# Performance work log

Measured on AMD Instinct MI355X. Metric: run time of the kernel, lower is better.

## Reference

```python
import jax, jax.numpy as jnp
import numpy as np

D_MODEL = 192
D_STATE = 16
D_CONV = 3
EXPAND = 2
D_INNER = EXPAND * D_MODEL
DT_RANK = (D_MODEL + 15) // 16  # ceil(d_model/16) = 12


def setup_inputs() -> dict:
    key = jax.random.key(0)
    ks = jax.random.split(key, 8)
    B, H, W = 4, 32, 32
    sc = lambda n: 1.0 / np.sqrt(n)
    x = jax.random.normal(ks[0], (B, H, W, D_MODEL), jnp.float32)
    W_in = jax.random.normal(ks[1], (D_MODEL, 2 * D_INNER), jnp.float32) * sc(D_MODEL)
    conv_w = jax.random.normal(ks[2], (D_INNER, 1, D_CONV, D_CONV), jnp.float32) * sc(D_CONV * D_CONV)
    conv_b = jnp.zeros((D_INNER,), jnp.float32)
    W_x = jax.random.normal(ks[3], (D_INNER, DT_RANK + 2 * D_STATE), jnp.float32) * sc(D_INNER)
    W_dt = jax.random.normal(ks[4], (DT_RANK, D_INNER), jnp.float32) * sc(DT_RANK)
    b_dt = jnp.zeros((D_INNER,), jnp.float32)
    A_log = jnp.log(jnp.tile(jnp.arange(1, D_STATE + 1, dtype=jnp.float32), (D_INNER, 1)))
    D_param = jnp.ones((D_INNER,), jnp.float32)
    W_out = jax.random.normal(ks[5], (D_INNER, D_MODEL), jnp.float32) * sc(D_INNER)
    gamma = jnp.ones((D_INNER,), jnp.float32)
    beta = jnp.zeros((D_INNER,), jnp.float32)
    return {"x": x, "W_in": W_in, "conv_w": conv_w, "conv_b": conv_b,
            "W_x": W_x, "W_dt": W_dt, "b_dt": b_dt, "A_log": A_log,
            "D_param": D_param, "W_out": W_out, "gamma": gamma, "beta": beta}


def _ssm_scan(u, W_x, W_dt, b_dt, A_log, D_param):
    # u: (B, L, D_inner). Log-cumsum closed-form linear SSM scan.
    x_dbl = u @ W_x                                   # (B,L,dt_rank+2N)
    dt = x_dbl[..., :DT_RANK]
    B_mat = x_dbl[..., DT_RANK:DT_RANK + D_STATE]     # (B,L,N)
    C_mat = x_dbl[..., DT_RANK + D_STATE:]            # (B,L,N)
    dt = jax.nn.softplus(dt @ W_dt + b_dt)            # (B,L,D)
    A = -jnp.exp(A_log)                               # (D,N)
    log_dA = jnp.einsum('bld,dn->bldn', dt, A)        # (B,L,D,N)
    dB_u = jnp.einsum('bld,bln->bldn', dt, B_mat) * u[..., None]
    log_decay = jnp.cumsum(log_dA, axis=1)
    decay = jnp.exp(log_decay)
    h = decay * jnp.cumsum(dB_u / (decay + 1e-12), axis=1)
    y = jnp.einsum('bldn,bln->bld', h, C_mat)
    return y + u * D_param


def reference(x, W_in, conv_w, conv_b, W_x, W_dt, b_dt, A_log, D_param, W_out, gamma, beta):
    B, H, W, C = x.shape
    xz = x @ W_in                                     # (B,H,W,2*D_inner)
    x_val, z = xz[..., :D_INNER], xz[..., D_INNER:]
    # depthwise 3x3 conv in NCHW
    xc = jnp.transpose(x_val, (0, 3, 1, 2))
    xc = jax.lax.conv_general_dilated(
        xc, conv_w, window_strides=(1, 1), padding='SAME',
        feature_group_count=D_INNER,
        dimension_numbers=('NCHW', 'OIHW', 'NCHW'))
    xc = xc + conv_b[None, :, None, None]
    xc = jax.nn.silu(xc)
    xv = jnp.transpose(xc, (0, 2, 3, 1))              # (B,H,W,D_inner)

    scan = lambda u: _ssm_scan(u, W_x, W_dt, b_dt, A_log, D_param)
    s1 = xv.reshape(B, H * W, D_INNER)                # row-major
    s2 = s1[:, ::-1]
    s3 = jnp.transpose(xv, (0, 2, 1, 3)).reshape(B, W * H, D_INNER)  # column-major
    s4 = s3[:, ::-1]
    y1 = scan(s1)
    y2 = scan(s2)[:, ::-1]
    y3 = scan(s3)
    y4 = scan(s4)[:, ::-1]
    # map column-major scans back to row-major order
    y3 = jnp.transpose(y3.reshape(B, W, H, D_INNER), (0, 2, 1, 3)).reshape(B, H * W, D_INNER)
    y4 = jnp.transpose(y4.reshape(B, W, H, D_INNER), (0, 2, 1, 3)).reshape(B, H * W, D_INNER)
    y = y1 + y2 + y3 + y4

    # LayerNorm over last dim (eps=1e-5)
    mu = jnp.mean(y, axis=-1, keepdims=True)
    var = jnp.mean(jnp.square(y - mu), axis=-1, keepdims=True)
    y = (y - mu) * jax.lax.rsqrt(var + 1e-5) * gamma + beta

    y = y.reshape(B, H, W, D_INNER) * jax.nn.silu(z)
    return y @ W_out
```

## Files before the change

kernel.cpp:

```cpp
#include <hip/hip_runtime.h>
#include <hip/hip_fp16.h>

#define DMODEL 192
#define DINNER 384
#define NPOS   4096
#define SEQL   1024
#define DSTATE 16
#define DTRANK 12

__device__ __forceinline__ float silu_f(float v) { return v * (1.f / (1.f + __expf(-v))); }

__device__ __forceinline__ int scan_pos(int dir, int l) {
    int s = (dir & 1) ? (SEQL - 1 - l) : l;
    return (dir & 2) ? (((s & 31) << 5) | (s >> 5)) : s;
}

__global__ void k1_inproj8(const float* __restrict__ x, const float* __restrict__ W_in,
                           float* __restrict__ x_val, float* __restrict__ gz) {
    __shared__ float xs[8 * DMODEL];
    const int t = threadIdx.x;
    const int pos0 = blockIdx.x << 3;
    for (int i = t; i < 8 * DMODEL; i += 384) xs[i] = x[pos0 * DMODEL + i];
    __syncthreads();

    float a0[8] = {0,0,0,0,0,0,0,0};
    float a1[8] = {0,0,0,0,0,0,0,0};
    for (int c = 0; c < DMODEL; ++c) {
        float w0 = W_in[c * 768 + t];
        float w1 = W_in[c * 768 + 384 + t];
#pragma unroll
        for (int g = 0; g < 8; ++g) {
            float xv = xs[g * DMODEL + c];
            a0[g] += w0 * xv;
            a1[g] += w1 * xv;
        }
    }
#pragma unroll
    for (int g = 0; g < 8; ++g) {
        x_val[(pos0 + g) * DINNER + t] = a0[g];
        gz[(pos0 + g) * DINNER + t]    = silu_f(a1[g]);
    }
}

__global__ void k2_conv(const float* __restrict__ x_val,
                        const float* __restrict__ conv_w, const float* __restrict__ conv_b,
                        const float* __restrict__ W_x,
                        __half* __restrict__ u_out, float* __restrict__ xd_out) {
    __shared__ float us[DINNER];
    __shared__ float part[8 * 44];
    const int t = threadIdx.x;
    const int pos = blockIdx.x;
    const int b = pos >> 10, hw = pos & 1023, h = hw >> 5, w = hw & 31;

    float acc = conv_b[t];
#pragma unroll
    for (int i = 0; i < 3; ++i) {
        int hh = h + i - 1;
        if (hh < 0 || hh > 31) continue;
#pragma unroll
        for (int j = 0; j < 3; ++j) {
            int ww = w + j - 1;
            if (ww < 0 || ww > 31) continue;
            acc += x_val[((b * 32 + hh) * 32 + ww) * DINNER + t] * conv_w[t * 9 + i * 3 + j];
        }
    }
    float uv = silu_f(acc);
    us[t] = uv;
    u_out[pos * DINNER + t] = __float2half(uv);
    __syncthreads();

    if (t < 352) {
        int o = t % 44, p = t / 44;
        float s = 0.f;
        int j0 = p * 48;
        for (int j = j0; j < j0 + 48; ++j) s += us[j] * W_x[j * 44 + o];
        part[p * 44 + o] = s;
    }
    __syncthreads();
    if (t < 44) {
        float s = 0.f;
#pragma unroll
        for (int p = 0; p < 8; ++p) s += part[p * 44 + t];
        xd_out[pos * 48 + t] = s;
    }
}

__global__ void k2c_dt_init(const float* __restrict__ xd, const float* __restrict__ W_dt,
                            const float* __restrict__ b_dt, const __half* __restrict__ u,
                            const float* __restrict__ Dp,
                            float* __restrict__ dt32, float* __restrict__ y_acc) {
    const int t = threadIdx.x;
    const int pos = blockIdx.x;
    const float* xr = xd + pos * 48;
    float raw = b_dt[t];
#pragma unroll
    for (int r = 0; r < DTRANK; ++r) raw += xr[r] * W_dt[r * DINNER + t];
    dt32[pos * DINNER + t] = fmaxf(raw, 0.f) + log1pf(__expf(-fabsf(raw)));

    y_acc[pos * DINNER + t] = 4.f * Dp[t] * __half2float(u[pos * DINNER + t]);
}

__global__ void k3_early(const __half* __restrict__ u, const float* __restrict__ xd,
                         const float* __restrict__ dt32, const float* __restrict__ A_log,
                         float* __restrict__ y_acc) {
    const int t = threadIdx.x;
    const int n = t & 15, dl = t >> 4;
    const int bi = blockIdx.x;
    const int chunk = bi % 24;
    const int b = (bi / 24) % 4;
    const int dir = bi / 96;
    const int d = chunk * 16 + dl;

    const float A = -__expf(A_log[d * DSTATE + n]);

    const __half* ub  = u    + b * SEQL * DINNER;
    const float* xb   = xd   + b * SEQL * 48;
    const float* dtb  = dt32 + b * SEQL * DINNER;
    float* yb = y_acc + b * SEQL * DINNER;

    float cum = 0.f, S = 0.f;
    for (int l0 = 0; l0 < SEQL; l0 += 8) {
        float dtv[8], Bv[8], Cv[8], uv[8];
        int   pk[8];
#pragma unroll
        for (int k = 0; k < 8; ++k) {
            int pos = scan_pos(dir, l0 + k);
            pk[k]  = pos;
            dtv[k] = dtb[pos * DINNER + d];
            Bv[k]  = xb[pos * 48 + DTRANK + n];
            Cv[k]  = xb[pos * 48 + DTRANK + DSTATE + n];
            uv[k]  = __half2float(ub[pos * DINNER + d]);
        }
#pragma unroll
        for (int k = 0; k < 8; ++k) {
            cum += dtv[k] * A;
            float decay = __expf(cum);
            S += (dtv[k] * Bv[k] * uv[k]) * __builtin_amdgcn_rcpf(decay + 1e-12f);
            float c = decay * S * Cv[k];
            c += __shfl_xor(c, 1);
            c += __shfl_xor(c, 2);
            c += __shfl_xor(c, 4);
            c += __shfl_xor(c, 8);
            if (n == 0) atomicAdd(&yb[pk[k] * DINNER + d], c);
        }
        if (__ballot(cum > -110.f) == 0ull) break;
    }
}

__global__ void k4_out4(const float* __restrict__ y_acc, const float* __restrict__ gz,
                        const float* __restrict__ gamma, const float* __restrict__ beta,
                        const float* __restrict__ W_out, float* __restrict__ out) {
    __shared__ float g_s[4 * DINNER];
    __shared__ float red[6];
    const int t = threadIdx.x;
    const int lane = t & 63, wave = t >> 6;
    const int pos0 = blockIdx.x << 2;

    const float g0c = gamma[t], g1c = gamma[t + 192];
    const float b0c = beta[t],  b1c = beta[t + 192];

    for (int p = 0; p < 4; ++p) {
        int pos = pos0 + p;
        float y0 = y_acc[pos * DINNER + t];
        float y1 = y_acc[pos * DINNER + t + 192];

        float s = y0 + y1;
#pragma unroll
        for (int off = 32; off > 0; off >>= 1) s += __shfl_xor(s, off);
        if (lane == 0) red[wave] = s;
        __syncthreads();
        float mu = (red[0] + red[1] + red[2]) * (1.f / 384.f);

        float d0 = y0 - mu, d1 = y1 - mu;
        float sq = d0 * d0 + d1 * d1;
#pragma unroll
        for (int off = 32; off > 0; off >>= 1) sq += __shfl_xor(sq, off);
        if (lane == 0) red[3 + wave] = sq;
        __syncthreads();
        float var = (red[3] + red[4] + red[5]) * (1.f / 384.f);
        float inv = rsqrtf(var + 1e-5f);

        g_s[p * DINNER + t]       = (d0 * inv * g0c + b0c) * gz[pos * DINNER + t];
        g_s[p * DINNER + t + 192] = (d1 * inv * g1c + b1c) * gz[pos * DINNER + t + 192];
        __syncthreads();
    }

    float acc[4] = {0.f, 0.f, 0.f, 0.f};
    for (int dd = 0; dd < DINNER; ++dd) {
        float w = W_out[dd * DMODEL + t];
#pragma unroll
        for (int p = 0; p < 4; ++p) acc[p] += g_s[p * DINNER + dd] * w;
    }
#pragma unroll
    for (int p = 0; p < 4; ++p) out[(pos0 + p) * DMODEL + t] = acc[p];
}

extern "C" void kernel_launch(void* const* d_in, const int* in_sizes, int n_in,
                              void* d_out, int out_size, void* d_ws, size_t ws_size,
                              hipStream_t stream) {
    (void)in_sizes; (void)n_in; (void)out_size; (void)ws_size;
    const float* x      = (const float*)d_in[0];
    const float* W_in   = (const float*)d_in[1];
    const float* conv_w = (const float*)d_in[2];
    const float* conv_b = (const float*)d_in[3];
    const float* W_x    = (const float*)d_in[4];
    const float* W_dt   = (const float*)d_in[5];
    const float* b_dt   = (const float*)d_in[6];
    const float* A_log  = (const float*)d_in[7];
    const float* Dp     = (const float*)d_in[8];
    const float* W_out  = (const float*)d_in[9];
    const float* gamma  = (const float*)d_in[10];
    const float* beta   = (const float*)d_in[11];

    char* base = (char*)d_ws;
    float*  R1   = (float*)base;
    __half* u    = (__half*)(base + 6291456);
    float*  xd   = (float*)(base + 9437184);
    float*  dt32 = (float*)(base + 10223616);
    float*  gz   = (float*)(base + 16515072);

    hipLaunchKernelGGL(k1_inproj8, dim3(NPOS / 8), dim3(384), 0, stream, x, W_in, R1, gz);
    hipLaunchKernelGGL(k2_conv, dim3(NPOS), dim3(384), 0, stream,
                       R1, conv_w, conv_b, W_x, u, xd);
    hipLaunchKernelGGL(k2c_dt_init, dim3(NPOS), dim3(384), 0, stream,
                       xd, W_dt, b_dt, u, Dp, dt32, R1);
    hipLaunchKernelGGL(k3_early, dim3(384), dim3(256), 0, stream,
                       u, xd, dt32, A_log, R1);
    hipLaunchKernelGGL(k4_out4, dim3(NPOS / 4), dim3(192), 0, stream,
                       R1, gz, gamma, beta, W_out, (float*)d_out);
}
```

Measured before the change: 233.1 us.

## Fuse dt/init into conv kernel, batch scan shuffles, widen output tiles

Merges the softplus dt projection and y_acc initialisation into the conv kernel, reusing the shared-memory xd row and the fp32 conv output instead of reloading from global memory, and moves y_acc to its own workspace buffer. This removes one launch and a global round-trip. The scan loop is split into phases so the exp/rcp and the cross-lane shuffle reductions for eight steps can interleave, and atomics are issued in a batch. The output kernel now handles 8 positions per block, reusing each W_out load across more rows at the cost of more registers and shared memory.

```diff
diff --git a/kernel.cpp b/kernel.cpp
--- a/kernel.cpp
+++ b/kernel.cpp
@@ -42,12 +42,15 @@
     }
 }
 
-__global__ void k2_conv(const float* __restrict__ x_val,
-                        const float* __restrict__ conv_w, const float* __restrict__ conv_b,
-                        const float* __restrict__ W_x,
-                        __half* __restrict__ u_out, float* __restrict__ xd_out) {
+__global__ void k2_conv_dt(const float* __restrict__ x_val,
+                           const float* __restrict__ conv_w, const float* __restrict__ conv_b,
+                           const float* __restrict__ W_x, const float* __restrict__ W_dt,
+                           const float* __restrict__ b_dt, const float* __restrict__ Dp,
+                           __half* __restrict__ u_out, float* __restrict__ xd_out,
+                           float* __restrict__ dt32, float* __restrict__ y_acc) {
     __shared__ float us[DINNER];
     __shared__ float part[8 * 44];
+    __shared__ float xdl[44];
     const int t = threadIdx.x;
     const int pos = blockIdx.x;
     const int b = pos >> 10, hw = pos & 1023, h = hw >> 5, w = hw & 31;
@@ -82,22 +85,16 @@
 #pragma unroll
         for (int p = 0; p < 8; ++p) s += part[p * 44 + t];
         xd_out[pos * 48 + t] = s;
-    }
-}
-
-__global__ void k2c_dt_init(const float* __restrict__ xd, const float* __restrict__ W_dt,
-                            const float* __restrict__ b_dt, const __half* __restrict__ u,
-                            const float* __restrict__ Dp,
-                            float* __restrict__ dt32, float* __restrict__ y_acc) {
-    const int t = threadIdx.x;
-    const int pos = blockIdx.x;
-    const float* xr = xd + pos * 48;
+        xdl[t] = s;
+    }
+    __syncthreads();
+
     float raw = b_dt[t];
 #pragma unroll
-    for (int r = 0; r < DTRANK; ++r) raw += xr[r] * W_dt[r * DINNER + t];
+    for (int r = 0; r < DTRANK; ++r) raw += xdl[r] * W_dt[r * DINNER + t];
     dt32[pos * DINNER + t] = fmaxf(raw, 0.f) + log1pf(__expf(-fabsf(raw)));
 
-    y_acc[pos * DINNER + t] = 4.f * Dp[t] * __half2float(u[pos * DINNER + t]);
+    y_acc[pos * DINNER + t] = 4.f * Dp[t] * uv;
 }
 
 __global__ void k3_early(const __half* __restrict__ u, const float* __restrict__ xd,
@@ -131,35 +128,44 @@
             Cv[k]  = xb[pos * 48 + DTRANK + DSTATE + n];
             uv[k]  = __half2float(ub[pos * DINNER + d]);
         }
+        float decay[8];
+#pragma unroll
+        for (int k = 0; k < 8; ++k) { cum += dtv[k] * A; decay[k] = __expf(cum); }
+        float rc[8];
+#pragma unroll
+        for (int k = 0; k < 8; ++k) rc[k] = __builtin_amdgcn_rcpf(decay[k] + 1e-12f);
+        float c[8];
 #pragma unroll
         for (int k = 0; k < 8; ++k) {
-            cum += dtv[k] * A;
-            float decay = __expf(cum);
-            S += (dtv[k] * Bv[k] * uv[k]) * __builtin_amdgcn_rcpf(decay + 1e-12f);
-            float c = decay * S * Cv[k];
-            c += __shfl_xor(c, 1);
-            c += __shfl_xor(c, 2);
-            c += __shfl_xor(c, 4);
-            c += __shfl_xor(c, 8);
-            if (n == 0) atomicAdd(&yb[pk[k] * DINNER + d], c);
+            S += (dtv[k] * Bv[k] * uv[k]) * rc[k];
+            c[k] = decay[k] * S * Cv[k];
+        }
+#pragma unroll
+        for (int off = 1; off <= 8; off <<= 1) {
+#pragma unroll
+            for (int k = 0; k < 8; ++k) c[k] += __shfl_xor(c[k], off);
+        }
+        if (n == 0) {
+#pragma unroll
+            for (int k = 0; k < 8; ++k) atomicAdd(&yb[pk[k] * DINNER + d], c[k]);
         }
         if (__ballot(cum > -110.f) == 0ull) break;
     }
 }
 
-__global__ void k4_out4(const float* __restrict__ y_acc, const float* __restrict__ gz,
+__global__ void k4_out8(const float* __restrict__ y_acc, const float* __restrict__ gz,
                         const float* __restrict__ gamma, const float* __restrict__ beta,
                         const float* __restrict__ W_out, float* __restrict__ out) {
-    __shared__ float g_s[4 * DINNER];
+    __shared__ float g_s[8 * DINNER];
     __shared__ float red[6];
     const int t = threadIdx.x;
     const int lane = t & 63, wave = t >> 6;
-    const int pos0 = blockIdx.x << 2;
+    const int pos0 = blockIdx.x << 3;
 
     const float g0c = gamma[t], g1c = gamma[t + 192];
     const float b0c = beta[t],  b1c = beta[t + 192];
 
-    for (int p = 0; p < 4; ++p) {
+    for (int p = 0; p < 8; ++p) {
         int pos = pos0 + p;
         float y0 = y_acc[pos * DINNER + t];
         float y1 = y_acc[pos * DINNER + t + 192];
@@ -185,14 +191,14 @@
         __syncthreads();
     }
 
-    float acc[4] = {0.f, 0.f, 0.f, 0.f};
+    float acc[8] = {0,0,0,0,0,0,0,0};
     for (int dd = 0; dd < DINNER; ++dd) {
         float w = W_out[dd * DMODEL + t];
 #pragma unroll
-        for (int p = 0; p < 4; ++p) acc[p] += g_s[p * DINNER + dd] * w;
-    }
-#pragma unroll
-    for (int p = 0; p < 4; ++p) out[(pos0 + p) * DMODEL + t] = acc[p];
+        for (int p = 0; p < 8; ++p) acc[p] += g_s[p * DINNER + dd] * w;
+    }
+#pragma unroll
+    for (int p = 0; p < 8; ++p) out[(pos0 + p) * DMODEL + t] = acc[p];
 }
 
 extern "C" void kernel_launch(void* const* d_in, const int* in_sizes, int n_in,
@@ -213,19 +219,18 @@
     const float* beta   = (const float*)d_in[11];
 
     char* base = (char*)d_ws;
-    float*  R1   = (float*)base;
-    __half* u    = (__half*)(base + 6291456);
-    float*  xd   = (float*)(base + 9437184);
-    float*  dt32 = (float*)(base + 10223616);
-    float*  gz   = (float*)(base + 16515072);
-
-    hipLaunchKernelGGL(k1_inproj8, dim3(NPOS / 8), dim3(384), 0, stream, x, W_in, R1, gz);
-    hipLaunchKernelGGL(k2_conv, dim3(NPOS), dim3(384), 0, stream,
-                       R1, conv_w, conv_b, W_x, u, xd);
-    hipLaunchKernelGGL(k2c_dt_init, dim3(NPOS), dim3(384), 0, stream,
-                       xd, W_dt, b_dt, u, Dp, dt32, R1);
+    float*  x_val = (float*)base;
+    __half* u     = (__half*)(base + 6291456);
+    float*  xd    = (float*)(base + 9437184);
+    float*  dt32  = (float*)(base + 10223616);
+    float*  gz    = (float*)(base + 16515072);
+    float*  y_acc = (float*)(base + 22806528);
+
+    hipLaunchKernelGGL(k1_inproj8, dim3(NPOS / 8), dim3(384), 0, stream, x, W_in, x_val, gz);
+    hipLaunchKernelGGL(k2_conv_dt, dim3(NPOS), dim3(384), 0, stream,
+                       x_val, conv_w, conv_b, W_x, W_dt, b_dt, Dp, u, xd, dt32, y_acc);
     hipLaunchKernelGGL(k3_early, dim3(384), dim3(256), 0, stream,
-                       u, xd, dt32, A_log, R1);
-    hipLaunchKernelGGL(k4_out4, dim3(NPOS / 4), dim3(192), 0, stream,
-                       R1, gz, gamma, beta, W_out, (float*)d_out);
-}
+                       u, xd, dt32, A_log, y_acc);
+    hipLaunchKernelGGL(k4_out8, dim3(NPOS / 8), dim3(192), 0, stream,
+                       y_acc, gz, gamma, beta, W_out, (float*)d_out);
+}
```

Measured after the change: 225.7 us. -3.2%, faster.
